# Performance work log

Measured on AMD Instinct MI355X. Metric: run time of the kernel, lower is better.

The kernel has to match this reference:

```python
import jax, jax.numpy as jnp
import numpy as np

B, S, D = 4, 2048, 1024

def setup_inputs() -> dict:
    key = jax.random.key(0)
    k1, k2, k3, k4 = jax.random.split(key, 4)
    scale = 1.0 / np.sqrt(D)
    x = jax.random.normal(k1, (B, S, D), dtype=jnp.float32)
    Wq = jax.random.normal(k2, (D, D), dtype=jnp.float32) * scale
    Wk = jax.random.normal(k3, (D, D), dtype=jnp.float32) * scale
    Wv = jax.random.normal(k4, (D, D), dtype=jnp.float32) * scale
    return {"x": x, "Wq": Wq, "Wk": Wk, "Wv": Wv}

def reference(x, Wq, Wk, Wv):
    # Linear projections (nn.Linear with bias=False computes x @ W.T)
    q = jnp.einsum('bsd,ed->bse', x, Wq)
    k = jnp.einsum('bsd,ed->bse', x, Wk)
    v = jnp.einsum('bsd,ed->bse', x, Wv)
    # HRR binding: circular convolution of k and v == elementwise product in FFT domain
    fq = jnp.fft.fft(q, axis=-1)
    fk = jnp.fft.fft(k, axis=-1)
    fv = jnp.fft.fft(v, axis=-1)
    # Causal associative memory: cumulative sum of bound key-value pairs over sequence
    mem = jnp.cumsum(fk * fv, axis=-2)  # [B, S, D] complex
    # Unbind with query via approximate inverse (complex conjugate of fft(q))
    out = jnp.fft.ifft(mem * jnp.conj(fq), axis=-1).real
    return out.astype(x.dtype)
```

## Files before the change

kernel.cpp:

```cpp
#include <hip/hip_runtime.h>

#define BB 4
#define SS 2048
#define DD 1024
#define MM 8192
#define CH 64
#define RR 32
#define PI_F 3.14159265358979323846f

typedef __attribute__((ext_vector_type(8))) short bf16x8;
typedef __attribute__((ext_vector_type(4))) float f32x4;

__device__ __forceinline__ unsigned short f2bf(float f) {
  unsigned int u = __float_as_uint(f);
  u = (u + 0x7FFFu + ((u >> 16) & 1u)) >> 16;
  return (unsigned short)u;
}
__device__ __forceinline__ float bf2f(unsigned short h) {
  return __uint_as_float(((unsigned int)h) << 16);
}

__global__ __launch_bounds__(256) void convert_bf16(
    const float* __restrict__ src, unsigned short* __restrict__ dst) {
  const long i = ((long)blockIdx.x * 256 + threadIdx.x) * 4;
  const float4 v = *(const float4*)&src[i];
  ushort4 o;
  o.x = f2bf(v.x); o.y = f2bf(v.y); o.z = f2bf(v.z); o.w = f2bf(v.w);
  *(ushort4*)&dst[i] = o;
}

__global__ __launch_bounds__(256) void convert_w(
    const float* __restrict__ Wq, const float* __restrict__ Wk,
    const float* __restrict__ Wv, unsigned short* __restrict__ dst) {
  const int z = blockIdx.y;
  const float* src = (z == 0) ? Wq : (z == 1) ? Wk : Wv;
  const long i = ((long)blockIdx.x * 256 + threadIdx.x) * 4;
  const float4 v = *(const float4*)&src[i];
  ushort4 o;
  o.x = f2bf(v.x); o.y = f2bf(v.y); o.z = f2bf(v.z); o.w = f2bf(v.w);
  *(ushort4*)&dst[(size_t)z * DD * DD + i] = o;
}

__device__ __forceinline__ void async16(const void* g, void* l) {
  __builtin_amdgcn_global_load_lds(
      (const __attribute__((address_space(1))) void*)g,
      (__attribute__((address_space(3))) void*)l, 16, 0, 0);
}

#define GW(n)  asm volatile("s_waitcnt vmcnt(" #n ")" ::: "memory")
#define LW()   do { asm volatile("s_waitcnt lgkmcnt(0)" ::: "memory"); \
                    __builtin_amdgcn_sched_barrier(0); } while (0)
#define BAR()  asm volatile("s_barrier" ::: "memory")

#define STA(buf, i, T) async16(xb + (size_t)(m0 + 64 * (i)) * DD + (T) * 64 + aOff, \
                               &Als[(buf) * 16384 + (i) * 4096 + slot8])
#define STB(buf, p, T) async16(W + (size_t)(n0 + 16 * (p)) * DD + (T) * 64 + bOff, \
                               &Bls[(buf) * 16384 + (p) * 4096 + slot8])
#define LDA(buf) { _Pragma("unroll") for (int mt = 0; mt < 8; ++mt) { \
    af[mt][0] = *(const bf16x8*)&Als[(buf) * 16384 + aRd + mt * 1024 + qoff0]; \
    af[mt][1] = *(const bf16x8*)&Als[(buf) * 16384 + aRd + mt * 1024 + qoff1]; } }
#define LDB(buf, p) { \
    bfv[0] = *(const bf16x8*)&Bls[(buf) * 16384 + (p) * 4096 + bRd + qoff0]; \
    bfv[1] = *(const bf16x8*)&Bls[(buf) * 16384 + (p) * 4096 + bRd + qoff1]; }
#define MMA(p) { __builtin_amdgcn_s_setprio(1); \
    _Pragma("unroll") for (int mt = 0; mt < 8; ++mt) { \
      acc[mt][p] = __builtin_amdgcn_mfma_f32_16x16x32_bf16(af[mt][0], bfv[0], acc[mt][p], 0, 0, 0); \
      acc[mt][p] = __builtin_amdgcn_mfma_f32_16x16x32_bf16(af[mt][1], bfv[1], acc[mt][p], 0, 0, 0); } \
    __builtin_amdgcn_s_setprio(0); }

__global__ __launch_bounds__(512, 2) void gemm_mfma(
    const unsigned short* __restrict__ xb,
    const unsigned short* __restrict__ Wb,
    float* __restrict__ outq, unsigned short* __restrict__ KV) {
  const int z = blockIdx.z;
  const unsigned short* W = Wb + (size_t)z * DD * DD;

  __shared__ unsigned short Als[2 * 16384];
  __shared__ unsigned short Bls[2 * 16384];

  const int tid  = threadIdx.x;
  const int lane = tid & 63;
  const int w    = tid >> 6;
  const int wm   = w >> 2;
  const int gq   = w & 3;
  const int fr   = lane & 15;
  const int kq   = lane >> 4;

  const int m0 = blockIdx.x * 256;
  const int n0 = blockIdx.y * 256;

  const int slot  = tid;
  const int srow  = slot >> 3;
  const int sq    = (slot & 7) ^ (srow & 7);
  const int slot8 = slot * 8;
  const size_t aOff = (size_t)srow * DD + sq * 8;
  const size_t bOff = (size_t)(64 * (slot >> 7) + ((slot >> 3) & 15)) * DD + sq * 8;

  const int qoff0 = ((0 + kq) ^ (fr & 7)) * 8;
  const int qoff1 = ((4 + kq) ^ (fr & 7)) * 8;
  const int aRd = wm * 8192 + fr * 64;
  const int bRd = gq * 1024 + fr * 64;

  f32x4 acc[8][4] = {};
  bf16x8 af[8][2];
  bf16x8 bfv[2];

  STA(0, 0, 0); STA(0, 1, 0);
  STA(0, 2, 0); STB(0, 0, 0);
  STA(0, 3, 0); STB(0, 1, 0);
  STB(0, 2, 0); STB(0, 3, 0);
  STA(1, 0, 1); STA(1, 1, 1);
  STA(1, 2, 1); STB(1, 0, 1);
  STA(1, 3, 1); STB(1, 1, 1);

  for (int T = 0; T < 14; ++T) {
    const int buf = T & 1;
    GW(9);  BAR(); LDA(buf); LDB(buf, 0);
    STB(buf ^ 1, 2, T + 1); STB(buf ^ 1, 3, T + 1); LW(); MMA(0);
    GW(10); BAR(); LDB(buf, 1);
    STA(buf, 0, T + 2); STA(buf, 1, T + 2);         LW(); MMA(1);
    GW(11); BAR(); LDB(buf, 2);
    STA(buf, 2, T + 2); STB(buf, 0, T + 2);         LW(); MMA(2);
    GW(12); BAR(); LDB(buf, 3);
    STA(buf, 3, T + 2); STB(buf, 1, T + 2);         LW(); MMA(3);
  }
  GW(9);  BAR(); LDA(0); LDB(0, 0); STB(1, 2, 15); STB(1, 3, 15); LW(); MMA(0);
  GW(10); BAR(); LDB(0, 1); LW(); MMA(1);
  GW(9);  BAR(); LDB(0, 2); LW(); MMA(2);
  GW(8);  BAR(); LDB(0, 3); LW(); MMA(3);
  GW(3);  BAR(); LDA(1); LDB(1, 0); LW(); MMA(0);
  GW(2);  BAR(); LDB(1, 1); LW(); MMA(1);
  GW(1);  BAR(); LDB(1, 2); LW(); MMA(2);
  GW(0);  BAR(); LDB(1, 3); LW(); MMA(3);

  const int col = lane & 15;
  const int r0  = (lane >> 4) * 4;
  const int mBase = m0 + wm * 128;
  const int nBase = n0 + gq * 64;
  if (z == 0) {
    #pragma unroll
    for (int mt = 0; mt < 8; ++mt)
      #pragma unroll
      for (int p = 0; p < 4; ++p)
        #pragma unroll
        for (int r = 0; r < 4; ++r)
          outq[(size_t)(mBase + mt * 16 + r0 + r) * DD + nBase + p * 16 + col] =
              acc[mt][p][r];
  } else {
    unsigned short* Ck = KV + (size_t)(z - 1) * DD;
    #pragma unroll
    for (int mt = 0; mt < 8; ++mt)
      #pragma unroll
      for (int p = 0; p < 4; ++p)
        #pragma unroll
        for (int r = 0; r < 4; ++r)
          Ck[(size_t)(mBase + mt * 16 + r0 + r) * 2048 + nBase + p * 16 + col] =
              f2bf(acc[mt][p][r]);
  }
}

__device__ __forceinline__ int pidx(int i) { return i + (i >> 6); }
#define BUFSZ 1040
__device__ __forceinline__ int pidx16(int i) { return i + (i >> 4); }
#define MEMSZ 546

__device__ __forceinline__ int rev4(int p) {
  unsigned r = __brev((unsigned)p) >> 22;
  return (int)(((r & 0x155u) << 1) | ((r & 0x2AAu) >> 1));
}

__host__ __device__ constexpr int clog2(int s) {
  return (s == 256) ? 8 : (s == 64) ? 6 : (s == 16) ? 4 : (s == 4) ? 2 : 0;
}

template <int S>
__device__ __forceinline__ void fwd_stage(float2 x[4], int t) {
  float c1 = 1.0f, s1 = 0.0f;
  if (S > 1) {
    const int j = t & (S - 1);
    __sincosf(-2.0f * PI_F * (float)j / (float)(4 * S), &s1, &c1);
  }
  const float c2 = c1 * c1 - s1 * s1, s2 = 2.0f * c1 * s1;
  const float c3 = c1 * c2 - s1 * s2, s3 = c1 * s2 + s1 * c2;
  const float Ar = x[0].x + x[2].x, Ai = x[0].y + x[2].y;
  const float Br = x[1].x + x[3].x, Bi = x[1].y + x[3].y;
  const float Cr = x[0].x - x[2].x, Ci = x[0].y - x[2].y;
  const float dr = x[1].x - x[3].x, di = x[1].y - x[3].y;
  const float y1r = Cr + di, y1i = Ci - dr;
  const float y2r = Ar - Br, y2i = Ai - Bi;
  const float y3r = Cr - di, y3i = Ci + dr;
  x[0] = make_float2(Ar + Br, Ai + Bi);
  x[1] = make_float2(y1r * c1 - y1i * s1, y1r * s1 + y1i * c1);
  x[2] = make_float2(y2r * c2 - y2i * s2, y2r * s2 + y2i * c2);
  x[3] = make_float2(y3r * c3 - y3i * s3, y3r * s3 + y3i * c3);
}

template <int S>
__device__ __forceinline__ void inv_stage(float2 x[4], int t) {
  float c1 = 1.0f, s1 = 0.0f;
  if (S > 1) {
    const int j = t & (S - 1);
    __sincosf(2.0f * PI_F * (float)j / (float)(4 * S), &s1, &c1);
  }
  const float c2 = c1 * c1 - s1 * s1, s2 = 2.0f * c1 * s1;
  const float c3 = c1 * c2 - s1 * s2, s3 = c1 * s2 + s1 * c2;
  const float u0r = x[0].x,                   u0i = x[0].y;
  const float u1r = x[1].x * c1 - x[1].y * s1, u1i = x[1].x * s1 + x[1].y * c1;
  const float u2r = x[2].x * c2 - x[2].y * s2, u2i = x[2].x * s2 + x[2].y * c2;
  const float u3r = x[3].x * c3 - x[3].y * s3, u3i = x[3].x * s3 + x[3].y * c3;
  const float Er = u0r + u2r, Ei = u0i + u2i;
  const float Fr = u0r - u2r, Fi = u0i - u2i;
  const float Gr = u1r + u3r, Gi = u1i + u3i;
  const float Hr = u1r - u3r, Hi = u1i - u3i;
  x[0] = make_float2(Er + Gr, Ei + Gi);
  x[1] = make_float2(Fr - Hi, Fi + Hr);
  x[2] = make_float2(Er - Gr, Ei - Gi);
  x[3] = make_float2(Fr + Hi, Fi - Hr);
}

template <int SW, int SR>
__device__ __forceinline__ void xchg(float2* buf, float2 x[4], int t) {
  constexpr int LW2 = clog2(SW), LR = clog2(SR);
  #pragma unroll
  for (int n = 0; n < 4; ++n)
    buf[pidx(((t >> LW2) << (LW2 + 2)) + (t & (SW - 1)) + n * SW)] = x[n];
  __syncthreads();
  #pragma unroll
  for (int n = 0; n < 4; ++n)
    x[n] = buf[pidx(((t >> LR) << (LR + 2)) + (t & (SR - 1)) + n * SR)];
  __syncthreads();
}

__device__ __forceinline__ void fwd_fft(float2* buf, float2 x[4], int t) {
  fwd_stage<256>(x, t); xchg<256, 64>(buf, x, t);
  fwd_stage<64>(x, t);  xchg<64, 16>(buf, x, t);
  fwd_stage<16>(x, t);  xchg<16, 4>(buf, x, t);
  fwd_stage<4>(x, t);   xchg<4, 1>(buf, x, t);
  fwd_stage<1>(x, t);
  #pragma unroll
  for (int n = 0; n < 4; ++n) buf[pidx(4 * t + n)] = x[n];
  __syncthreads();
}

__global__ __launch_bounds__(256) void bind_kernel(unsigned short* __restrict__ KV) {
  __shared__ float2 buf[BUFSZ];
  const int t = threadIdx.x;
  unsigned short* row = KV + (long)blockIdx.x * 2048;

  float2 x[4];
  #pragma unroll
  for (int n = 0; n < 4; ++n) {
    const int i = t + 256 * n;
    x[n] = make_float2(bf2f(row[i]), bf2f(row[1024 + i]));
  }
  fwd_fft(buf, x, t);

  float2* Prow = (float2*)row;
  #pragma unroll
  for (int m = 0; m < 2; ++m) {
    const int s = t + 256 * m;
    if (s == 0) {
      const float2 W0   = buf[pidx(0)];
      const float2 W512 = buf[pidx(2)];
      Prow[0] = make_float2(W0.x * W0.y, W512.x * W512.y);
    } else {
      const int p1 = rev4(s);
      const int p2 = rev4(1024 - s);
      const float2 F1 = buf[pidx(p1)], F2 = buf[pidx(p2)];
      const float fkr = 0.5f * (F1.x + F2.x), fki = 0.5f * (F1.y - F2.y);
      const float fvr = 0.5f * (F1.y + F2.y), fvi = 0.5f * (F2.x - F1.x);
      Prow[s] = make_float2(fkr * fvr - fki * fvi, fkr * fvi + fki * fvr);
    }
  }
}

__global__ __launch_bounds__(256) void scan_chunk_sum(
    const float2* __restrict__ P, float2* __restrict__ csum) {
  const int chunk = blockIdx.x;
  const int batch = blockIdx.y >> 1;
  const int f = (blockIdx.y & 1) * 256 + threadIdx.x;
  long base = ((long)batch * SS + (long)chunk * RR) * 512 + f;
  float sr = 0.0f, si = 0.0f;
  #pragma unroll 4
  for (int i = 0; i < RR; ++i) {
    float2 p = P[base + (long)i * 512];
    sr += p.x; si += p.y;
  }
  csum[((long)batch * CH + chunk) * 512 + f] = make_float2(sr, si);
}

__global__ __launch_bounds__(256) void scan_chunk_scan(float2* csum) {
  const int idx = blockIdx.x * 256 + threadIdx.x;
  const int batch = idx >> 9;
  const int f = idx & 511;
  float2 v[CH];
  #pragma unroll
  for (int c = 0; c < CH; ++c) v[c] = csum[((long)batch * CH + c) * 512 + f];
  float rr = 0.0f, ri = 0.0f;
  #pragma unroll
  for (int c = 0; c < CH; ++c) {
    const float2 x = v[c];
    csum[((long)batch * CH + c) * 512 + f] = make_float2(rr, ri);
    rr += x.x; ri += x.y;
  }
}

__global__ __launch_bounds__(256) void scan_apply(
    float2* __restrict__ P, const float2* __restrict__ csum) {
  const int chunk = blockIdx.x;
  const int batch = blockIdx.y >> 1;
  const int f = (blockIdx.y & 1) * 256 + threadIdx.x;
  float2 off = csum[((long)batch * CH + chunk) * 512 + f];
  float ar = off.x, ai = off.y;
  long base = ((long)batch * SS + (long)chunk * RR) * 512 + f;
  for (int i = 0; i < RR; ++i) {
    const long o = base + (long)i * 512;
    float2 p = P[o];
    ar += p.x; ai += p.y;
    P[o] = make_float2(ar, ai);
  }
}

__global__ __launch_bounds__(256) void unbind_kernel(
    float* __restrict__ qout, const float2* __restrict__ mem) {
  __shared__ float2 buf[BUFSZ];
  __shared__ float2 m0s[MEMSZ], m1s[MEMSZ];
  const int t = threadIdx.x;
  const long r0 = (long)blockIdx.x * 2;
  float* row0 = qout + r0 * DD;
  float* row1 = row0 + DD;
  const float2* mem0 = mem + r0 * 512;
  const float2* mem1 = mem0 + 512;

  float2 x[4];
  #pragma unroll
  for (int n = 0; n < 4; ++n) {
    const int i = t + 256 * n;
    x[n] = make_float2(row0[i], row1[i]);
  }
  #pragma unroll
  for (int n = 0; n < 2; ++n) {
    const int s = t + 256 * n;
    const float2 a = mem0[s], b = mem1[s];
    if (s == 0) {
      m0s[pidx16(0)]   = make_float2(a.x, 0.0f);
      m0s[pidx16(512)] = make_float2(a.y, 0.0f);
      m1s[pidx16(0)]   = make_float2(b.x, 0.0f);
      m1s[pidx16(512)] = make_float2(b.y, 0.0f);
    } else {
      m0s[pidx16(s)] = a;
      m1s[pidx16(s)] = b;
    }
  }
  fwd_fft(buf, x, t);

  float2 z[4];
  #pragma unroll
  for (int m = 0; m < 4; ++m) {
    const int p   = t + 256 * m;
    const int bin = rev4(p);
    const int p2  = rev4((1024 - bin) & 1023);
    const float2 F1 = buf[pidx(p)], F2 = buf[pidx(p2)];
    const float q0r = 0.5f * (F1.x + F2.x), q0i = 0.5f * (F1.y - F2.y);
    const float q1r = 0.5f * (F1.y + F2.y), q1i = 0.5f * (F2.x - F1.x);
    const int  ix = (bin <= 512) ? bin : 1024 - bin;
    const float sg = (bin <= 512) ? 1.0f : -1.0f;
    float2 m0 = m0s[pidx16(ix)], m1 = m1s[pidx16(ix)];
    m0.y *= sg; m1.y *= sg;
    const float z0r = m0.x * q0r + m0.y * q0i, z0i = m0.y * q0r - m0.x * q0i;
    const float z1r = m1.x * q1r + m1.y * q1i, z1i = m1.y * q1r - m1.x * q1i;
    z[m] = make_float2(z0r - z1i, z0i + z1r);
  }
  __syncthreads();
  #pragma unroll
  for (int m = 0; m < 4; ++m) buf[pidx(t + 256 * m)] = z[m];
  __syncthreads();
  #pragma unroll
  for (int n = 0; n < 4; ++n) x[n] = buf[pidx(4 * t + n)];

  inv_stage<1>(x, t);   xchg<1, 4>(buf, x, t);
  inv_stage<4>(x, t);   xchg<4, 16>(buf, x, t);
  inv_stage<16>(x, t);  xchg<16, 64>(buf, x, t);
  inv_stage<64>(x, t);  xchg<64, 256>(buf, x, t);
  inv_stage<256>(x, t);

  const float sc = 1.0f / 1024.0f;
  #pragma unroll
  for (int n = 0; n < 4; ++n) {
    const int i = t + 256 * n;
    row0[i] = x[n].x * sc;
    row1[i] = x[n].y * sc;
  }
}

extern "C" void kernel_launch(void* const* d_in, const int* in_sizes, int n_in,
                              void* d_out, int out_size, void* d_ws, size_t ws_size,
                              hipStream_t stream) {
  (void)in_sizes; (void)n_in; (void)out_size;
  const float* x  = (const float*)d_in[0];
  const float* Wq = (const float*)d_in[1];
  const float* Wk = (const float*)d_in[2];
  const float* Wv = (const float*)d_in[3];
  float* out = (float*)d_out;

  const size_t wbytes = (size_t)3 * DD * DD * 2;
  auto need = [&](size_t MHr, size_t nB) {
    return wbytes + MHr * DD * 2 + MHr * 4096 + nB * CH * 512 * 8;
  };
  const int nPass = (ws_size >= need(8192, 4)) ? 1 : 2;
  const size_t MH = MM / nPass;
  const int    nB = BB / nPass;

  char* ws = (char*)d_ws;
  unsigned short* Wb = (unsigned short*)ws;
  unsigned short* xb = (unsigned short*)(ws + wbytes);
  unsigned short* KV = (unsigned short*)(ws + wbytes + MH * DD * 2);
  float2*       csum = (float2*)((char*)KV + MH * 4096);

  convert_w<<<dim3(DD * DD / 1024, 3), 256, 0, stream>>>(Wq, Wk, Wv, Wb);

  for (int h = 0; h < nPass; ++h) {
    const float* xh   = x   + (size_t)h * MH * DD;
    float*       outh = out + (size_t)h * MH * DD;

    convert_bf16<<<MH * DD / 1024, 256, 0, stream>>>(xh, xb);
    gemm_mfma<<<dim3(MH / 256, DD / 256, 3), dim3(512), 0, stream>>>(xb, Wb, outh, KV);
    bind_kernel<<<MH, 256, 0, stream>>>(KV);
    scan_chunk_sum<<<dim3(CH, nB * 2), 256, 0, stream>>>((const float2*)KV, csum);
    scan_chunk_scan<<<nB * 2, 256, 0, stream>>>(csum);
    scan_apply<<<dim3(CH, nB * 2), 256, 0, stream>>>((float2*)KV, csum);
    unbind_kernel<<<MH / 2, 256, 0, stream>>>(outh, (const float2*)KV);
  }
}
```

Before: 238.6 us.

## Restructure GEMM main loop to load all B fragments and stream A in pairs

Reorders the bf16 MFMA GEMM inner pipeline. Each tile now loads all four B fragments up front and streams A fragments two m-tiles at a time, instead of loading all eight A fragments and one B fragment per phase. The async global-to-LDS prefetch order and waitcnt/barrier placement are reworked to match. The aim is fewer live A registers, which may help occupancy, and better overlap of LDS reads with MFMA. In exchange it adds extra barriers per phase and more delicate vmcnt accounting that could stall or race.

```diff
diff --git a/kernel.cpp b/kernel.cpp
--- a/kernel.cpp
+++ b/kernel.cpp
@@ -48,6 +48,7 @@
 }
 
 #define GW(n)  asm volatile("s_waitcnt vmcnt(" #n ")" ::: "memory")
+#define LT8()  asm volatile("s_waitcnt lgkmcnt(8)" ::: "memory")
 #define LW()   do { asm volatile("s_waitcnt lgkmcnt(0)" ::: "memory"); \
                     __builtin_amdgcn_sched_barrier(0); } while (0)
 #define BAR()  asm volatile("s_barrier" ::: "memory")
@@ -56,17 +57,21 @@
                                &Als[(buf) * 16384 + (i) * 4096 + slot8])
 #define STB(buf, p, T) async16(W + (size_t)(n0 + 16 * (p)) * DD + (T) * 64 + bOff, \
                                &Bls[(buf) * 16384 + (p) * 4096 + slot8])
-#define LDA(buf) { _Pragma("unroll") for (int mt = 0; mt < 8; ++mt) { \
-    af[mt][0] = *(const bf16x8*)&Als[(buf) * 16384 + aRd + mt * 1024 + qoff0]; \
-    af[mt][1] = *(const bf16x8*)&Als[(buf) * 16384 + aRd + mt * 1024 + qoff1]; } }
-#define LDB(buf, p) { \
-    bfv[0] = *(const bf16x8*)&Bls[(buf) * 16384 + (p) * 4096 + bRd + qoff0]; \
-    bfv[1] = *(const bf16x8*)&Bls[(buf) * 16384 + (p) * 4096 + bRd + qoff1]; }
-#define MMA(p) { __builtin_amdgcn_s_setprio(1); \
-    _Pragma("unroll") for (int mt = 0; mt < 8; ++mt) { \
-      acc[mt][p] = __builtin_amdgcn_mfma_f32_16x16x32_bf16(af[mt][0], bfv[0], acc[mt][p], 0, 0, 0); \
-      acc[mt][p] = __builtin_amdgcn_mfma_f32_16x16x32_bf16(af[mt][1], bfv[1], acc[mt][p], 0, 0, 0); } \
-    __builtin_amdgcn_s_setprio(0); }
+
+#define LDA2(buf, q) { _Pragma("unroll") for (int j = 0; j < 2; ++j) { \
+    af[j][0] = *(const bf16x8*)&Als[(buf) * 16384 + aRd + (2 * (q) + j) * 1024 + qoff0]; \
+    af[j][1] = *(const bf16x8*)&Als[(buf) * 16384 + aRd + (2 * (q) + j) * 1024 + qoff1]; } }
+#define LDBALL(buf) { _Pragma("unroll") for (int p = 0; p < 4; ++p) { \
+    bfv[p][0] = *(const bf16x8*)&Bls[(buf) * 16384 + (p) * 4096 + bRd + qoff0]; \
+    bfv[p][1] = *(const bf16x8*)&Bls[(buf) * 16384 + (p) * 4096 + bRd + qoff1]; } }
+#define MMA2(q) { __builtin_amdgcn_s_setprio(1); \
+    _Pragma("unroll") for (int j = 0; j < 2; ++j) \
+      _Pragma("unroll") for (int p = 0; p < 4; ++p) { \
+        acc[2 * (q) + j][p] = __builtin_amdgcn_mfma_f32_16x16x32_bf16( \
+            af[j][0], bfv[p][0], acc[2 * (q) + j][p], 0, 0, 0); \
+        acc[2 * (q) + j][p] = __builtin_amdgcn_mfma_f32_16x16x32_bf16( \
+            af[j][1], bfv[p][1], acc[2 * (q) + j][p], 0, 0, 0); } \
+    __builtin_amdgcn_s_setprio(0); __builtin_amdgcn_sched_barrier(0); }
 
 __global__ __launch_bounds__(512, 2) void gemm_mfma(
     const unsigned short* __restrict__ xb,
@@ -102,36 +107,46 @@
   const int bRd = gq * 1024 + fr * 64;
 
   f32x4 acc[8][4] = {};
-  bf16x8 af[8][2];
-  bf16x8 bfv[2];
-
-  STA(0, 0, 0); STA(0, 1, 0);
-  STA(0, 2, 0); STB(0, 0, 0);
-  STA(0, 3, 0); STB(0, 1, 0);
-  STB(0, 2, 0); STB(0, 3, 0);
-  STA(1, 0, 1); STA(1, 1, 1);
-  STA(1, 2, 1); STB(1, 0, 1);
-  STA(1, 3, 1); STB(1, 1, 1);
+  bf16x8 af[2][2];
+  bf16x8 bfv[4][2];
+
+  STA(0, 0, 0); STA(0, 2, 0);
+  STB(0, 0, 0); STB(0, 1, 0); STB(0, 2, 0); STB(0, 3, 0);
+  STA(0, 1, 0); STA(0, 3, 0);
+  STA(1, 0, 1); STA(1, 2, 1);
+  STB(1, 0, 1); STB(1, 1, 1); STB(1, 2, 1); STB(1, 3, 1);
+  GW(8); BAR();
 
   for (int T = 0; T < 14; ++T) {
     const int buf = T & 1;
-    GW(9);  BAR(); LDA(buf); LDB(buf, 0);
-    STB(buf ^ 1, 2, T + 1); STB(buf ^ 1, 3, T + 1); LW(); MMA(0);
-    GW(10); BAR(); LDB(buf, 1);
-    STA(buf, 0, T + 2); STA(buf, 1, T + 2);         LW(); MMA(1);
-    GW(11); BAR(); LDB(buf, 2);
-    STA(buf, 2, T + 2); STB(buf, 0, T + 2);         LW(); MMA(2);
-    GW(12); BAR(); LDB(buf, 3);
-    STA(buf, 3, T + 2); STB(buf, 1, T + 2);         LW(); MMA(3);
-  }
-  GW(9);  BAR(); LDA(0); LDB(0, 0); STB(1, 2, 15); STB(1, 3, 15); LW(); MMA(0);
-  GW(10); BAR(); LDB(0, 1); LW(); MMA(1);
-  GW(9);  BAR(); LDB(0, 2); LW(); MMA(2);
-  GW(8);  BAR(); LDB(0, 3); LW(); MMA(3);
-  GW(3);  BAR(); LDA(1); LDB(1, 0); LW(); MMA(0);
-  GW(2);  BAR(); LDB(1, 1); LW(); MMA(1);
-  GW(1);  BAR(); LDB(1, 2); LW(); MMA(2);
-  GW(0);  BAR(); LDB(1, 3); LW(); MMA(3);
+    LDBALL(buf); LDA2(buf, 0);
+    STA(buf ^ 1, 1, T + 1); STA(buf ^ 1, 3, T + 1);
+    LT8();
+    BAR(); LW(); MMA2(0); BAR();
+    GW(8);
+    LDA2(buf, 1);
+    STB(buf, 0, T + 2); STB(buf, 1, T + 2);
+    BAR(); LW(); MMA2(1); BAR();
+    LDA2(buf, 2);
+    STB(buf, 2, T + 2); STB(buf, 3, T + 2);
+    BAR(); LW(); MMA2(2); BAR();
+    GW(6);
+    LDA2(buf, 3);
+    STA(buf, 0, T + 2); STA(buf, 2, T + 2);
+    BAR(); LW(); MMA2(3); BAR();
+  }
+
+  LDBALL(0); LDA2(0, 0);
+  STA(1, 1, 15); STA(1, 3, 15);
+  LT8();
+  BAR(); LW(); MMA2(0); BAR();
+  GW(8); LDA2(0, 1); BAR(); LW(); MMA2(1); BAR();
+  LDA2(0, 2); BAR(); LW(); MMA2(2); BAR();
+  GW(2); LDA2(0, 3); BAR(); LW(); MMA2(3); BAR();
+  LDBALL(1); LDA2(1, 0); BAR(); LW(); MMA2(0); BAR();
+  GW(0); LDA2(1, 1); BAR(); LW(); MMA2(1); BAR();
+  LDA2(1, 2); BAR(); LW(); MMA2(2); BAR();
+  LDA2(1, 3); LW(); MMA2(3);
 
   const int col = lane & 15;
   const int r0  = (lane >> 4) * 4;
```

New measurement: 241.5 us. About the same (+1.2%).

## Double-buffer B fragments in GEMM mainloop and batch loads in scan kernels

Applied to the files above, without the earlier changes.

The GEMM mainloop now keeps two register banks for B fragments, so the LDS read for the next sub-tile is issued before the MFMA block on the current one. The explicit lgkmcnt waits are dropped, and the vmcnt wait now happens once per K-step instead of once per sub-step, relying on the compiler's own waits. The scan chunk-sum and apply kernels now load 8 rows at a time into registers to put more memory requests in flight. This costs extra VGPRs and relaxes the async-load wait discipline, which could expose races or lower occupancy.

```diff
diff --git a/kernel.cpp b/kernel.cpp
--- a/kernel.cpp
+++ b/kernel.cpp
@@ -48,9 +48,8 @@
 }
 
 #define GW(n)  asm volatile("s_waitcnt vmcnt(" #n ")" ::: "memory")
-#define LW()   do { asm volatile("s_waitcnt lgkmcnt(0)" ::: "memory"); \
-                    __builtin_amdgcn_sched_barrier(0); } while (0)
 #define BAR()  asm volatile("s_barrier" ::: "memory")
+#define SB0()  __builtin_amdgcn_sched_barrier(0)
 
 #define STA(buf, i, T) async16(xb + (size_t)(m0 + 64 * (i)) * DD + (T) * 64 + aOff, \
                                &Als[(buf) * 16384 + (i) * 4096 + slot8])
@@ -59,13 +58,13 @@
 #define LDA(buf) { _Pragma("unroll") for (int mt = 0; mt < 8; ++mt) { \
     af[mt][0] = *(const bf16x8*)&Als[(buf) * 16384 + aRd + mt * 1024 + qoff0]; \
     af[mt][1] = *(const bf16x8*)&Als[(buf) * 16384 + aRd + mt * 1024 + qoff1]; } }
-#define LDB(buf, p) { \
-    bfv[0] = *(const bf16x8*)&Bls[(buf) * 16384 + (p) * 4096 + bRd + qoff0]; \
-    bfv[1] = *(const bf16x8*)&Bls[(buf) * 16384 + (p) * 4096 + bRd + qoff1]; }
-#define MMA(p) { __builtin_amdgcn_s_setprio(1); \
+#define LDB(buf, p, bank) { \
+    bank[0] = *(const bf16x8*)&Bls[(buf) * 16384 + (p) * 4096 + bRd + qoff0]; \
+    bank[1] = *(const bf16x8*)&Bls[(buf) * 16384 + (p) * 4096 + bRd + qoff1]; }
+#define MMA(p, bank) { __builtin_amdgcn_s_setprio(1); \
     _Pragma("unroll") for (int mt = 0; mt < 8; ++mt) { \
-      acc[mt][p] = __builtin_amdgcn_mfma_f32_16x16x32_bf16(af[mt][0], bfv[0], acc[mt][p], 0, 0, 0); \
-      acc[mt][p] = __builtin_amdgcn_mfma_f32_16x16x32_bf16(af[mt][1], bfv[1], acc[mt][p], 0, 0, 0); } \
+      acc[mt][p] = __builtin_amdgcn_mfma_f32_16x16x32_bf16(af[mt][0], bank[0], acc[mt][p], 0, 0, 0); \
+      acc[mt][p] = __builtin_amdgcn_mfma_f32_16x16x32_bf16(af[mt][1], bank[1], acc[mt][p], 0, 0, 0); } \
     __builtin_amdgcn_s_setprio(0); }
 
 __global__ __launch_bounds__(512, 2) void gemm_mfma(
@@ -103,7 +102,7 @@
 
   f32x4 acc[8][4] = {};
   bf16x8 af[8][2];
-  bf16x8 bfv[2];
+  bf16x8 bva[2], bvb[2];
 
   STA(0, 0, 0); STA(0, 1, 0);
   STA(0, 2, 0); STB(0, 0, 0);
@@ -115,23 +114,37 @@
 
   for (int T = 0; T < 14; ++T) {
     const int buf = T & 1;
-    GW(9);  BAR(); LDA(buf); LDB(buf, 0);
-    STB(buf ^ 1, 2, T + 1); STB(buf ^ 1, 3, T + 1); LW(); MMA(0);
-    GW(10); BAR(); LDB(buf, 1);
-    STA(buf, 0, T + 2); STA(buf, 1, T + 2);         LW(); MMA(1);
-    GW(11); BAR(); LDB(buf, 2);
-    STA(buf, 2, T + 2); STB(buf, 0, T + 2);         LW(); MMA(2);
-    GW(12); BAR(); LDB(buf, 3);
-    STA(buf, 3, T + 2); STB(buf, 1, T + 2);         LW(); MMA(3);
-  }
-  GW(9);  BAR(); LDA(0); LDB(0, 0); STB(1, 2, 15); STB(1, 3, 15); LW(); MMA(0);
-  GW(10); BAR(); LDB(0, 1); LW(); MMA(1);
-  GW(9);  BAR(); LDB(0, 2); LW(); MMA(2);
-  GW(8);  BAR(); LDB(0, 3); LW(); MMA(3);
-  GW(3);  BAR(); LDA(1); LDB(1, 0); LW(); MMA(0);
-  GW(2);  BAR(); LDB(1, 1); LW(); MMA(1);
-  GW(1);  BAR(); LDB(1, 2); LW(); MMA(2);
-  GW(0);  BAR(); LDB(1, 3); LW(); MMA(3);
+    SB0(); GW(6); BAR();
+    LDA(buf); LDB(buf, 0, bva);
+    STB(buf ^ 1, 2, T + 1); STB(buf ^ 1, 3, T + 1);
+    LDB(buf, 1, bvb);
+    MMA(0, bva);
+    SB0(); BAR();
+    STA(buf, 0, T + 2); STA(buf, 1, T + 2);
+    LDB(buf, 2, bva);
+    MMA(1, bvb);
+    SB0(); BAR();
+    STA(buf, 2, T + 2); STB(buf, 0, T + 2);
+    LDB(buf, 3, bvb);
+    MMA(2, bva);
+    SB0(); BAR();
+    STA(buf, 3, T + 2); STB(buf, 1, T + 2);
+    MMA(3, bvb);
+  }
+  SB0(); GW(6); BAR();
+  LDA(0); LDB(0, 0, bva);
+  STB(1, 2, 15); STB(1, 3, 15);
+  LDB(0, 1, bvb);
+  MMA(0, bva);
+  SB0(); BAR(); LDB(0, 2, bva); MMA(1, bvb);
+  SB0(); BAR(); LDB(0, 3, bvb); MMA(2, bva);
+  SB0(); BAR(); MMA(3, bvb);
+  SB0(); GW(0); BAR();
+  LDA(1); LDB(1, 0, bva); LDB(1, 1, bvb);
+  MMA(0, bva);
+  SB0(); BAR(); LDB(1, 2, bva); MMA(1, bvb);
+  SB0(); BAR(); LDB(1, 3, bvb); MMA(2, bva);
+  SB0(); BAR(); MMA(3, bvb);
 
   const int col = lane & 15;
   const int r0  = (lane >> 4) * 4;
@@ -281,10 +294,13 @@
   const int f = (blockIdx.y & 1) * 256 + threadIdx.x;
   long base = ((long)batch * SS + (long)chunk * RR) * 512 + f;
   float sr = 0.0f, si = 0.0f;
-  #pragma unroll 4
-  for (int i = 0; i < RR; ++i) {
-    float2 p = P[base + (long)i * 512];
-    sr += p.x; si += p.y;
+  #pragma unroll
+  for (int i0 = 0; i0 < RR; i0 += 8) {
+    float2 p[8];
+    #pragma unroll
+    for (int j = 0; j < 8; ++j) p[j] = P[base + (long)(i0 + j) * 512];
+    #pragma unroll
+    for (int j = 0; j < 8; ++j) { sr += p[j].x; si += p[j].y; }
   }
   csum[((long)batch * CH + chunk) * 512 + f] = make_float2(sr, si);
 }
@@ -313,11 +329,16 @@
   float2 off = csum[((long)batch * CH + chunk) * 512 + f];
   float ar = off.x, ai = off.y;
   long base = ((long)batch * SS + (long)chunk * RR) * 512 + f;
-  for (int i = 0; i < RR; ++i) {
-    const long o = base + (long)i * 512;
-    float2 p = P[o];
-    ar += p.x; ai += p.y;
-    P[o] = make_float2(ar, ai);
+  #pragma unroll
+  for (int i0 = 0; i0 < RR; i0 += 8) {
+    float2 p[8];
+    #pragma unroll
+    for (int j = 0; j < 8; ++j) p[j] = P[base + (long)(i0 + j) * 512];
+    #pragma unroll
+    for (int j = 0; j < 8; ++j) {
+      ar += p[j].x; ai += p[j].y;
+      P[base + (long)(i0 + j) * 512] = make_float2(ar, ai);
+    }
   }
 }
 
```

Result: faster. 233.5 us (-2.1%).
